# Kernel tuning notes

Measured on AMD Instinct MI355X. Metric: run time of the kernel, lower is better.

The kernel has to match this reference:

```python
import jax, jax.numpy as jnp
from jax import lax
import numpy as np

B, T, E, D, U = 64, 2048, 512, 1024, 128


def setup_inputs() -> dict:
    key = jax.random.key(0)
    ks = jax.random.split(key, 12)
    s = 0.05
    queries = jax.random.normal(ks[0], (B, 1, D), jnp.float32)
    prev = jax.random.uniform(ks[1], (B, T), jnp.float32)
    prev = prev / prev.sum(-1, keepdims=True)  # alignment-like (sums to 1)
    enc = jax.random.normal(ks[2], (B, T, E), jnp.float32)
    lengths = jax.random.randint(ks[3], (B,), 1, T + 1)
    conv_w = jax.random.normal(ks[4], (U, 1, 3), jnp.float32) * s   # (out,in,k)
    conv_b = jax.random.normal(ks[5], (U,), jnp.float32) * s
    Wq = jax.random.normal(ks[6], (U, D), jnp.float32) * s          # query_layer weight
    Wk = jax.random.normal(ks[7], (U, E), jnp.float32) * s          # key_layer weight
    v_w = jax.random.normal(ks[8], (1, U), jnp.float32) * s         # v weight
    v_b = jax.random.normal(ks[9], (1,), jnp.float32) * s           # v bias
    b = jax.random.uniform(ks[10], (U,), jnp.float32)               # nn.Parameter(torch.rand)
    return dict(queries=queries, previous_alignments=prev, encoder_output=enc,
                conv_w=conv_w, conv_b=conv_b, Wq=Wq, Wk=Wk, v_w=v_w, v_b=v_b,
                b=b, lengths=lengths)


def reference(queries, previous_alignments, encoder_output, conv_w, conv_b,
              Wq, Wk, v_w, v_b, b, lengths):
    Bt, Tt, Et = encoder_output.shape
    # set_memory: proj_key and mask
    proj_key = jnp.einsum('bte,ue->btu', encoder_output, Wk)          # (B,T,U)
    mask = jnp.arange(Tt)[None, :] >= lengths[:, None]                # (B,T)
    # conv1d on previous alignments, kernel 3, padding 1
    conv = lax.conv_general_dilated(previous_alignments[:, None, :], conv_w,
                                    window_strides=(1,), padding=[(1, 1)],
                                    dimension_numbers=('NCH', 'OIH', 'NCH'))
    conv_attn = (conv + conv_b[None, :, None]).transpose(0, 2, 1)     # (B,T,U)
    q_proj = jnp.einsum('bqd,ud->bqu', queries, Wq)                   # (B,1,U)
    w = jnp.tanh(q_proj + proj_key + conv_attn + b)                   # (B,T,U)
    score = jnp.einsum('btu,u->bt', w, v_w[0]) + v_b[0]               # (B,T)
    score = jnp.where(mask, -jnp.inf, score)
    attn_weight = jax.nn.softmax(score, axis=-1)                      # (B,T)
    context = jnp.einsum('bt,bte->be', attn_weight, encoder_output)[:, None, :]  # (B,1,E)
    return context, attn_weight
```

## Files before the change

### kernel.cpp

```cpp
#include <hip/hip_runtime.h>
#include <hip/hip_bf16.h>

typedef __bf16 bf16x8 __attribute__((ext_vector_type(8)));
typedef float  f32x4  __attribute__((ext_vector_type(4)));

#define Bsz 64
#define Tdim 2048
#define Edim 512
#define Ddim 1024
#define Udim 128
#define CHUNK 128
#define NCHUNK 16

__device__ inline unsigned short f2bf(float f) {
    union { float f; unsigned int u; } x{f};
    unsigned int r = x.u + 0x7FFFu + ((x.u >> 16) & 1u);
    return (unsigned short)(r >> 16);
}

__device__ inline float fast_tanh(float x) {
    float e = __expf(2.f * x);
    return 1.f - __fdividef(2.f, e + 1.f);
}

__global__ __launch_bounds__(256) void k_prep(const float* __restrict__ q,
                                              const float* __restrict__ Wq,
                                              const float* __restrict__ bparam,
                                              const float* __restrict__ convb,
                                              const float* __restrict__ Wk,
                                              unsigned short* __restrict__ wkbf,
                                              float* __restrict__ qb) {
    int bid = blockIdx.x, tid = threadIdx.x;
    if (bid >= 512) {
        int cb = bid - 512;
        #pragma unroll
        for (int k = 0; k < 4; ++k) {
            int i = (((cb * 4 + k) * 256) + tid) * 4;
            float4 v = *reinterpret_cast<const float4*>(Wk + i);
            ushort4 h = make_ushort4(f2bf(v.x), f2bf(v.y), f2bf(v.z), f2bf(v.w));
            *reinterpret_cast<ushort4*>(wkbf + i) = h;
        }
        return;
    }
    int wg   = bid * 4 + (tid >> 6);
    int lane = tid & 63;
    int b  = wg >> 5;
    int u0 = (wg & 31) * 4;
    const float* qr = q + (size_t)b * Ddim + lane * 16;
    float4 qv[4];
    #pragma unroll
    for (int i = 0; i < 4; ++i) qv[i] = *reinterpret_cast<const float4*>(qr + i * 4);
    float s[4];
    #pragma unroll
    for (int jj = 0; jj < 4; ++jj) {
        const float* wr = Wq + (size_t)(u0 + jj) * Ddim + lane * 16;
        float acc = 0.f;
        #pragma unroll
        for (int i = 0; i < 4; ++i) {
            float4 w = *reinterpret_cast<const float4*>(wr + i * 4);
            acc += qv[i].x * w.x + qv[i].y * w.y + qv[i].z * w.z + qv[i].w * w.w;
        }
        s[jj] = acc;
    }
    #pragma unroll
    for (int m = 32; m; m >>= 1) {
        #pragma unroll
        for (int jj = 0; jj < 4; ++jj) s[jj] += __shfl_xor(s[jj], m);
    }
    if (lane == 0) {
        #pragma unroll
        for (int jj = 0; jj < 4; ++jj)
            qb[b * 128 + u0 + jj] = s[jj] + bparam[u0 + jj] + convb[u0 + jj];
    }
}

__global__ __launch_bounds__(256) void k_score_ctx(const float* __restrict__ enc,
                                                   const float* __restrict__ prev,
                                                   const unsigned short* __restrict__ wkbf,
                                                   const float* __restrict__ qb,
                                                   const float* __restrict__ conv_w,
                                                   const float* __restrict__ v_w,
                                                   const float* __restrict__ v_b,
                                                   const int* __restrict__ lengths,
                                                   float* __restrict__ score_out,
                                                   float* __restrict__ m_ws,
                                                   float* __restrict__ l_ws,
                                                   float* __restrict__ c_ws) {
    __shared__ alignas(16) unsigned short At[128 * 64];
    __shared__ alignas(16) unsigned short Bt[128 * 64];
    __shared__ float s_prev[130];
    __shared__ float s_qb[128];
    __shared__ float s_vw[128];
    __shared__ float s_cw[3][128];
    __shared__ float s_score[128];
    __shared__ float s_p[128];
    __shared__ alignas(16) float s_cred[128 * 4];

    const int tid   = threadIdx.x;
    const int b     = blockIdx.y;
    const int chunk = blockIdx.x;
    const int t0    = chunk * CHUNK;
    const int lane  = tid & 63, wid = tid >> 6;
    const int len   = lengths[b];
    const int pidx  = b * NCHUNK + chunk;

    if (t0 >= len) {
        if (tid == 0) { m_ws[pidx] = -3.4e38f; l_ws[pidx] = 0.f; }
        return;
    }

    if (tid < 128) {
        s_qb[tid]    = qb[b * 128 + tid];
        s_vw[tid]    = v_w[tid];
        s_cw[0][tid] = conv_w[tid * 3 + 0];
        s_cw[1][tid] = conv_w[tid * 3 + 1];
        s_cw[2][tid] = conv_w[tid * 3 + 2];
    }
    if (tid < 130) {
        int idx = t0 - 1 + tid;
        s_prev[tid] = (idx >= 0 && idx < Tdim) ? prev[b * Tdim + idx] : 0.f;
    }

    const float* encb = enc + ((size_t)b * Tdim + t0) * Edim;

    f32x4 acc[2][8];
    #pragma unroll
    for (int m2 = 0; m2 < 2; ++m2)
        #pragma unroll
        for (int n = 0; n < 8; ++n) acc[m2][n] = (f32x4){0.f, 0.f, 0.f, 0.f};

    for (int e0 = 0; e0 < Edim; e0 += 64) {
        #pragma unroll
        for (int i = 0; i < 8; ++i) {
            int lin = tid + i * 256;
            int r = lin >> 4, c4 = lin & 15;
            float4 v = *reinterpret_cast<const float4*>(encb + (size_t)r * Edim + e0 + c4 * 4);
            ushort4 h = make_ushort4(f2bf(v.x), f2bf(v.y), f2bf(v.z), f2bf(v.w));
            int off = (r * 128 + c4 * 8) ^ ((r & 7) << 4);
            *reinterpret_cast<ushort4*>(reinterpret_cast<char*>(At) + off) = h;
        }
        #pragma unroll
        for (int i = 0; i < 4; ++i) {
            int lin = tid + i * 256;
            int u = lin >> 3, c8 = lin & 7;
            uint4 w = *reinterpret_cast<const uint4*>(wkbf + (size_t)u * Edim + e0 + c8 * 8);
            int off = (u * 128 + c8 * 16) ^ ((u & 7) << 4);
            *reinterpret_cast<uint4*>(reinterpret_cast<char*>(Bt) + off) = w;
        }
        __syncthreads();
        #pragma unroll
        for (int kk = 0; kk < 2; ++kk) {
            #pragma unroll
            for (int m2 = 0; m2 < 2; ++m2) {
                int ar = wid * 32 + m2 * 16 + (lane & 15);
                int abyte = (ar * 128 + kk * 64 + (lane >> 4) * 16) ^ ((ar & 7) << 4);
                bf16x8 af = *reinterpret_cast<const bf16x8*>(reinterpret_cast<const char*>(At) + abyte);
                #pragma unroll
                for (int n = 0; n < 8; ++n) {
                    int br = n * 16 + (lane & 15);
                    int bbyte = (br * 128 + kk * 64 + (lane >> 4) * 16) ^ ((br & 7) << 4);
                    bf16x8 bv = *reinterpret_cast<const bf16x8*>(reinterpret_cast<const char*>(Bt) + bbyte);
                    acc[m2][n] = __builtin_amdgcn_mfma_f32_16x16x32_bf16(af, bv, acc[m2][n], 0, 0, 0);
                }
            }
        }
        __syncthreads();
    }

    float sc[2][4] = {{0.f,0.f,0.f,0.f},{0.f,0.f,0.f,0.f}};
    #pragma unroll
    for (int m2 = 0; m2 < 2; ++m2) {
        #pragma unroll
        for (int n = 0; n < 8; ++n) {
            int u = n * 16 + (lane & 15);
            float c0 = s_cw[0][u], c1 = s_cw[1][u], c2 = s_cw[2][u];
            float qbu = s_qb[u], vwu = s_vw[u];
            #pragma unroll
            for (int j = 0; j < 4; ++j) {
                int tl = wid * 32 + m2 * 16 + (lane >> 4) * 4 + j;
                float conv = s_prev[tl] * c0 + s_prev[tl + 1] * c1 + s_prev[tl + 2] * c2;
                sc[m2][j] += vwu * fast_tanh(acc[m2][n][j] + qbu + conv);
            }
        }
    }
    #pragma unroll
    for (int m2 = 0; m2 < 2; ++m2)
        #pragma unroll
        for (int j = 0; j < 4; ++j) {
            sc[m2][j] += __shfl_xor(sc[m2][j], 1);
            sc[m2][j] += __shfl_xor(sc[m2][j], 2);
            sc[m2][j] += __shfl_xor(sc[m2][j], 4);
            sc[m2][j] += __shfl_xor(sc[m2][j], 8);
        }
    if ((lane & 15) == 0) {
        float vb = v_b[0];
        #pragma unroll
        for (int m2 = 0; m2 < 2; ++m2) {
            int tl = wid * 32 + m2 * 16 + (lane >> 4) * 4;
            #pragma unroll
            for (int j = 0; j < 4; ++j) {
                float s = sc[m2][j] + vb;
                s_score[tl + j] = s;
                score_out[b * Tdim + t0 + tl + j] = s;
            }
        }
    }
    __syncthreads();

    float sv0 = (t0 + lane < len)      ? s_score[lane]      : -3.4e38f;
    float sv1 = (t0 + 64 + lane < len) ? s_score[lane + 64] : -3.4e38f;
    float m = fmaxf(sv0, sv1);
    #pragma unroll
    for (int s = 32; s; s >>= 1) m = fmaxf(m, __shfl_xor(m, s));
    float p0 = (t0 + lane < len)      ? __expf(sv0 - m) : 0.f;
    float p1 = (t0 + 64 + lane < len) ? __expf(sv1 - m) : 0.f;
    float l = p0 + p1;
    #pragma unroll
    for (int s = 32; s; s >>= 1) l += __shfl_xor(l, s);
    if (tid < 64) { s_p[tid] = p0; s_p[tid + 64] = p1; }
    if (tid == 0) { m_ws[pidx] = m; l_ws[pidx] = l; }
    __syncthreads();

    {
        int e4 = (tid & 127) * 4;
        int th = tid >> 7;
        float4 a = make_float4(0.f, 0.f, 0.f, 0.f);
        #pragma unroll 4
        for (int t = th; t < CHUNK; t += 2) {
            float pt = s_p[t];
            float4 v = *reinterpret_cast<const float4*>(encb + (size_t)t * Edim + e4);
            a.x += pt * v.x; a.y += pt * v.y; a.z += pt * v.z; a.w += pt * v.w;
        }
        if (th == 1) *reinterpret_cast<float4*>(&s_cred[(tid & 127) * 4]) = a;
        __syncthreads();
        if (th == 0) {
            float4 o = *reinterpret_cast<const float4*>(&s_cred[tid * 4]);
            a.x += o.x; a.y += o.y; a.z += o.z; a.w += o.w;
            *reinterpret_cast<float4*>(c_ws + (size_t)pidx * Edim + e4) = a;
        }
    }
}

__global__ __launch_bounds__(256) void k_combine(const float* __restrict__ m_ws,
                                                 const float* __restrict__ l_ws,
                                                 const float* __restrict__ c_ws,
                                                 const int* __restrict__ lengths,
                                                 float* __restrict__ ctx,
                                                 float* __restrict__ attn) {
    int b = blockIdx.x, tid = threadIdx.x;
    int lane = tid & 63, wid = tid >> 6;
    __shared__ float s_w[NCHUNK];
    __shared__ float sM, sinvL;

    if (wid == 0) {
        float mj = (lane < NCHUNK) ? m_ws[b * NCHUNK + lane] : -3.4e38f;
        float lj = (lane < NCHUNK) ? l_ws[b * NCHUNK + lane] : 0.f;
        float M = mj;
        #pragma unroll
        for (int s = 32; s; s >>= 1) M = fmaxf(M, __shfl_xor(M, s));
        float w = (lj > 0.f) ? __expf(mj - M) : 0.f;
        float L = lj * w;
        #pragma unroll
        for (int s = 32; s; s >>= 1) L += __shfl_xor(L, s);
        if (lane < NCHUNK) s_w[lane] = w;
        if (lane == 0) { sM = M; sinvL = 1.f / L; }
    }
    __syncthreads();
    float M = sM, invL = sinvL;

    {
        int e2 = tid * 2;
        float ax = 0.f, ay = 0.f;
        #pragma unroll 4
        for (int j = 0; j < NCHUNK; ++j) {
            float w = s_w[j];
            if (w != 0.f) {
                float2 v = *reinterpret_cast<const float2*>(c_ws + ((size_t)(b * NCHUNK + j)) * Edim + e2);
                ax += w * v.x; ay += w * v.y;
            }
        }
        float2 r = make_float2(ax * invL, ay * invL);
        *reinterpret_cast<float2*>(ctx + (size_t)b * Edim + e2) = r;
    }

    int len = lengths[b];
    #pragma unroll
    for (int i = 0; i < Tdim / 256; ++i) {
        int t = tid + i * 256;
        float s = attn[(size_t)b * Tdim + t];
        attn[(size_t)b * Tdim + t] = (t < len) ? __expf(s - M) * invL : 0.f;
    }
}

extern "C" void kernel_launch(void* const* d_in, const int* in_sizes, int n_in,
                              void* d_out, int out_size, void* d_ws, size_t ws_size,
                              hipStream_t stream) {
    const float* queries = (const float*)d_in[0];
    const float* prev    = (const float*)d_in[1];
    const float* enc     = (const float*)d_in[2];
    const float* conv_w  = (const float*)d_in[3];
    const float* conv_b  = (const float*)d_in[4];
    const float* Wq      = (const float*)d_in[5];
    const float* Wk      = (const float*)d_in[6];
    const float* v_w     = (const float*)d_in[7];
    const float* v_b     = (const float*)d_in[8];
    const float* bparam  = (const float*)d_in[9];
    const int*   lengths = (const int*)d_in[10];

    float* out  = (float*)d_out;
    float* ctx  = out;
    float* attn = out + Bsz * Edim;

    char* ws = (char*)d_ws;
    unsigned short* wkbf = (unsigned short*)ws;
    float* qb   = (float*)(ws + 131072);
    float* m_ws = (float*)(ws + 163840);
    float* l_ws = (float*)(ws + 172032);
    float* c_ws = (float*)(ws + 196608);

    k_prep<<<528, 256, 0, stream>>>(queries, Wq, bparam, conv_b, Wk, wkbf, qb);
    k_score_ctx<<<dim3(NCHUNK, Bsz), 256, 0, stream>>>(enc, prev, wkbf, qb, conv_w, v_w, v_b,
                                                       lengths, attn, m_ws, l_ws, c_ws);
    k_combine<<<Bsz, 256, 0, stream>>>(m_ws, l_ws, c_ws, lengths, ctx, attn);
}
```

Measured before the change: 80.35 us.

## Double time chunk per block and use native bf16 conversions

Each score/context block now covers 256 time steps instead of 128, with a 4x8 MFMA accumulator tile per wave. This halves the number of blocks and the redundant Wk tile staging per time step. The manual round-to-nearest bf16 bit trick is replaced by native __bf16 casts, which can map to hardware convert instructions. The prep kernel's query projection now computes 8 units per wave with fewer blocks. The cost is more registers per thread and coarser skipping of masked chunks, which may reduce occupancy and add wasted work past each sequence length.

```diff
diff --git a/kernel.cpp b/kernel.cpp
--- a/kernel.cpp
+++ b/kernel.cpp
@@ -2,6 +2,7 @@
 #include <hip/hip_bf16.h>
 
 typedef __bf16 bf16x8 __attribute__((ext_vector_type(8)));
+typedef __bf16 bf16x4 __attribute__((ext_vector_type(4)));
 typedef float  f32x4  __attribute__((ext_vector_type(4)));
 
 #define Bsz 64
@@ -9,13 +10,13 @@
 #define Edim 512
 #define Ddim 1024
 #define Udim 128
-#define CHUNK 128
-#define NCHUNK 16
-
-__device__ inline unsigned short f2bf(float f) {
-    union { float f; unsigned int u; } x{f};
-    unsigned int r = x.u + 0x7FFFu + ((x.u >> 16) & 1u);
-    return (unsigned short)(r >> 16);
+#define CHUNK 256
+#define NCHUNK 8
+
+__device__ inline bf16x4 cvt4(float4 v) {
+    bf16x4 h;
+    h[0] = (__bf16)v.x; h[1] = (__bf16)v.y; h[2] = (__bf16)v.z; h[3] = (__bf16)v.w;
+    return h;
 }
 
 __device__ inline float fast_tanh(float x) {
@@ -31,28 +32,27 @@
                                               unsigned short* __restrict__ wkbf,
                                               float* __restrict__ qb) {
     int bid = blockIdx.x, tid = threadIdx.x;
-    if (bid >= 512) {
-        int cb = bid - 512;
+    if (bid >= 256) {
+        int cb = bid - 256;
         #pragma unroll
         for (int k = 0; k < 4; ++k) {
             int i = (((cb * 4 + k) * 256) + tid) * 4;
             float4 v = *reinterpret_cast<const float4*>(Wk + i);
-            ushort4 h = make_ushort4(f2bf(v.x), f2bf(v.y), f2bf(v.z), f2bf(v.w));
-            *reinterpret_cast<ushort4*>(wkbf + i) = h;
+            *reinterpret_cast<bf16x4*>(wkbf + i) = cvt4(v);
         }
         return;
     }
     int wg   = bid * 4 + (tid >> 6);
     int lane = tid & 63;
-    int b  = wg >> 5;
-    int u0 = (wg & 31) * 4;
+    int b  = wg >> 4;
+    int u0 = (wg & 15) * 8;
     const float* qr = q + (size_t)b * Ddim + lane * 16;
     float4 qv[4];
     #pragma unroll
     for (int i = 0; i < 4; ++i) qv[i] = *reinterpret_cast<const float4*>(qr + i * 4);
-    float s[4];
-    #pragma unroll
-    for (int jj = 0; jj < 4; ++jj) {
+    float s[8];
+    #pragma unroll
+    for (int jj = 0; jj < 8; ++jj) {
         const float* wr = Wq + (size_t)(u0 + jj) * Ddim + lane * 16;
         float acc = 0.f;
         #pragma unroll
@@ -65,11 +65,11 @@
     #pragma unroll
     for (int m = 32; m; m >>= 1) {
         #pragma unroll
-        for (int jj = 0; jj < 4; ++jj) s[jj] += __shfl_xor(s[jj], m);
+        for (int jj = 0; jj < 8; ++jj) s[jj] += __shfl_xor(s[jj], m);
     }
     if (lane == 0) {
         #pragma unroll
-        for (int jj = 0; jj < 4; ++jj)
+        for (int jj = 0; jj < 8; ++jj)
             qb[b * 128 + u0 + jj] = s[jj] + bparam[u0 + jj] + convb[u0 + jj];
     }
 }
@@ -86,14 +86,14 @@
                                                    float* __restrict__ m_ws,
                                                    float* __restrict__ l_ws,
                                                    float* __restrict__ c_ws) {
-    __shared__ alignas(16) unsigned short At[128 * 64];
+    __shared__ alignas(16) unsigned short At[256 * 64];
     __shared__ alignas(16) unsigned short Bt[128 * 64];
-    __shared__ float s_prev[130];
+    __shared__ float s_prev[258];
     __shared__ float s_qb[128];
     __shared__ float s_vw[128];
     __shared__ float s_cw[3][128];
-    __shared__ float s_score[128];
-    __shared__ float s_p[128];
+    __shared__ float s_score[256];
+    __shared__ float s_p[256];
     __shared__ alignas(16) float s_cred[128 * 4];
 
     const int tid   = threadIdx.x;
@@ -116,28 +116,32 @@
         s_cw[1][tid] = conv_w[tid * 3 + 1];
         s_cw[2][tid] = conv_w[tid * 3 + 2];
     }
-    if (tid < 130) {
+    if (tid < 258 - 128 && tid + 128 < 258) {}
+    if (tid < 258) {
         int idx = t0 - 1 + tid;
         s_prev[tid] = (idx >= 0 && idx < Tdim) ? prev[b * Tdim + idx] : 0.f;
     }
+    if (tid < 2) {
+        int idx = t0 - 1 + 256 + tid;
+        s_prev[256 + tid] = (idx >= 0 && idx < Tdim) ? prev[b * Tdim + idx] : 0.f;
+    }
 
     const float* encb = enc + ((size_t)b * Tdim + t0) * Edim;
 
-    f32x4 acc[2][8];
-    #pragma unroll
-    for (int m2 = 0; m2 < 2; ++m2)
+    f32x4 acc[4][8];
+    #pragma unroll
+    for (int m2 = 0; m2 < 4; ++m2)
         #pragma unroll
         for (int n = 0; n < 8; ++n) acc[m2][n] = (f32x4){0.f, 0.f, 0.f, 0.f};
 
     for (int e0 = 0; e0 < Edim; e0 += 64) {
         #pragma unroll
-        for (int i = 0; i < 8; ++i) {
+        for (int i = 0; i < 16; ++i) {
             int lin = tid + i * 256;
             int r = lin >> 4, c4 = lin & 15;
             float4 v = *reinterpret_cast<const float4*>(encb + (size_t)r * Edim + e0 + c4 * 4);
-            ushort4 h = make_ushort4(f2bf(v.x), f2bf(v.y), f2bf(v.z), f2bf(v.w));
             int off = (r * 128 + c4 * 8) ^ ((r & 7) << 4);
-            *reinterpret_cast<ushort4*>(reinterpret_cast<char*>(At) + off) = h;
+            *reinterpret_cast<bf16x4*>(reinterpret_cast<char*>(At) + off) = cvt4(v);
         }
         #pragma unroll
         for (int i = 0; i < 4; ++i) {
@@ -151,8 +155,8 @@
         #pragma unroll
         for (int kk = 0; kk < 2; ++kk) {
             #pragma unroll
-            for (int m2 = 0; m2 < 2; ++m2) {
-                int ar = wid * 32 + m2 * 16 + (lane & 15);
+            for (int m2 = 0; m2 < 4; ++m2) {
+                int ar = wid * 64 + m2 * 16 + (lane & 15);
                 int abyte = (ar * 128 + kk * 64 + (lane >> 4) * 16) ^ ((ar & 7) << 4);
                 bf16x8 af = *reinterpret_cast<const bf16x8*>(reinterpret_cast<const char*>(At) + abyte);
                 #pragma unroll
@@ -167,9 +171,13 @@
         __syncthreads();
     }
 
-    float sc[2][4] = {{0.f,0.f,0.f,0.f},{0.f,0.f,0.f,0.f}};
-    #pragma unroll
-    for (int m2 = 0; m2 < 2; ++m2) {
+    float sc[4][4];
+    #pragma unroll
+    for (int m2 = 0; m2 < 4; ++m2)
+        #pragma unroll
+        for (int j = 0; j < 4; ++j) sc[m2][j] = 0.f;
+    #pragma unroll
+    for (int m2 = 0; m2 < 4; ++m2) {
         #pragma unroll
         for (int n = 0; n < 8; ++n) {
             int u = n * 16 + (lane & 15);
@@ -177,14 +185,14 @@
             float qbu = s_qb[u], vwu = s_vw[u];
             #pragma unroll
             for (int j = 0; j < 4; ++j) {
-                int tl = wid * 32 + m2 * 16 + (lane >> 4) * 4 + j;
+                int tl = wid * 64 + m2 * 16 + (lane >> 4) * 4 + j;
                 float conv = s_prev[tl] * c0 + s_prev[tl + 1] * c1 + s_prev[tl + 2] * c2;
                 sc[m2][j] += vwu * fast_tanh(acc[m2][n][j] + qbu + conv);
             }
         }
     }
     #pragma unroll
-    for (int m2 = 0; m2 < 2; ++m2)
+    for (int m2 = 0; m2 < 4; ++m2)
         #pragma unroll
         for (int j = 0; j < 4; ++j) {
             sc[m2][j] += __shfl_xor(sc[m2][j], 1);
@@ -195,8 +203,8 @@
     if ((lane & 15) == 0) {
         float vb = v_b[0];
         #pragma unroll
-        for (int m2 = 0; m2 < 2; ++m2) {
-            int tl = wid * 32 + m2 * 16 + (lane >> 4) * 4;
+        for (int m2 = 0; m2 < 4; ++m2) {
+            int tl = wid * 64 + m2 * 16 + (lane >> 4) * 4;
             #pragma unroll
             for (int j = 0; j < 4; ++j) {
                 float s = sc[m2][j] + vb;
@@ -207,17 +215,27 @@
     }
     __syncthreads();
 
-    float sv0 = (t0 + lane < len)      ? s_score[lane]      : -3.4e38f;
-    float sv1 = (t0 + 64 + lane < len) ? s_score[lane + 64] : -3.4e38f;
-    float m = fmaxf(sv0, sv1);
+    float sv[4], pv[4];
+    float m = -3.4e38f;
+    #pragma unroll
+    for (int h = 0; h < 4; ++h) {
+        sv[h] = (t0 + h * 64 + lane < len) ? s_score[h * 64 + lane] : -3.4e38f;
+        m = fmaxf(m, sv[h]);
+    }
     #pragma unroll
     for (int s = 32; s; s >>= 1) m = fmaxf(m, __shfl_xor(m, s));
-    float p0 = (t0 + lane < len)      ? __expf(sv0 - m) : 0.f;
-    float p1 = (t0 + 64 + lane < len) ? __expf(sv1 - m) : 0.f;
-    float l = p0 + p1;
+    float l = 0.f;
+    #pragma unroll
+    for (int h = 0; h < 4; ++h) {
+        pv[h] = (t0 + h * 64 + lane < len) ? __expf(sv[h] - m) : 0.f;
+        l += pv[h];
+    }
     #pragma unroll
     for (int s = 32; s; s >>= 1) l += __shfl_xor(l, s);
-    if (tid < 64) { s_p[tid] = p0; s_p[tid + 64] = p1; }
+    if (tid < 64) {
+        #pragma unroll
+        for (int h = 0; h < 4; ++h) s_p[h * 64 + tid] = pv[h];
+    }
     if (tid == 0) { m_ws[pidx] = m; l_ws[pidx] = l; }
     __syncthreads();
 
@@ -271,7 +289,7 @@
     {
         int e2 = tid * 2;
         float ax = 0.f, ay = 0.f;
-        #pragma unroll 4
+        #pragma unroll
         for (int j = 0; j < NCHUNK; ++j) {
             float w = s_w[j];
             if (w != 0.f) {
@@ -318,7 +336,7 @@
     float* l_ws = (float*)(ws + 172032);
     float* c_ws = (float*)(ws + 196608);
 
-    k_prep<<<528, 256, 0, stream>>>(queries, Wq, bparam, conv_b, Wk, wkbf, qb);
+    k_prep<<<272, 256, 0, stream>>>(queries, Wq, bparam, conv_b, Wk, wkbf, qb);
     k_score_ctx<<<dim3(NCHUNK, Bsz), 256, 0, stream>>>(enc, prev, wkbf, qb, conv_w, v_w, v_b,
                                                        lengths, attn, m_ws, l_ws, c_ws);
     k_combine<<<Bsz, 256, 0, stream>>>(m_ws, l_ws, c_ws, lengths, ctx, attn);
```

New measurement: 108.7 us. 1.35x slower.

## Pre-swizzle Wk into MFMA fragment layout and read B operands from global

Applied to the files above, without the earlier changes.

The prep kernel now writes the bf16 copy of Wk directly in the per-lane MFMA B-fragment order. The score kernel loads B fragments straight from global/L2 instead of staging them in shared memory, which removes the Bt LDS buffer and its stores. Encoder loads are widened to 8 floats per thread with compiler bf16 conversion, and the q-projection uses 8 outputs per wave. This saves LDS traffic and space but depends on L2 hits for the repeated Wk fragment reads across blocks.

```diff
diff --git a/kernel.cpp b/kernel.cpp
--- a/kernel.cpp
+++ b/kernel.cpp
@@ -2,6 +2,7 @@
 #include <hip/hip_bf16.h>
 
 typedef __bf16 bf16x8 __attribute__((ext_vector_type(8)));
+typedef __bf16 bf16x4 __attribute__((ext_vector_type(4)));
 typedef float  f32x4  __attribute__((ext_vector_type(4)));
 
 #define Bsz 64
@@ -12,10 +13,16 @@
 #define CHUNK 128
 #define NCHUNK 16
 
-__device__ inline unsigned short f2bf(float f) {
-    union { float f; unsigned int u; } x{f};
-    unsigned int r = x.u + 0x7FFFu + ((x.u >> 16) & 1u);
-    return (unsigned short)(r >> 16);
+__device__ inline bf16x4 cvt4(float4 v) {
+    bf16x4 h;
+    h[0] = (__bf16)v.x; h[1] = (__bf16)v.y; h[2] = (__bf16)v.z; h[3] = (__bf16)v.w;
+    return h;
+}
+__device__ inline bf16x8 cvt8(float4 a, float4 b) {
+    bf16x8 h;
+    h[0] = (__bf16)a.x; h[1] = (__bf16)a.y; h[2] = (__bf16)a.z; h[3] = (__bf16)a.w;
+    h[4] = (__bf16)b.x; h[5] = (__bf16)b.y; h[6] = (__bf16)b.z; h[7] = (__bf16)b.w;
+    return h;
 }
 
 __device__ inline float fast_tanh(float x) {
@@ -31,28 +38,35 @@
                                               unsigned short* __restrict__ wkbf,
                                               float* __restrict__ qb) {
     int bid = blockIdx.x, tid = threadIdx.x;
-    if (bid >= 512) {
-        int cb = bid - 512;
-        #pragma unroll
-        for (int k = 0; k < 4; ++k) {
-            int i = (((cb * 4 + k) * 256) + tid) * 4;
-            float4 v = *reinterpret_cast<const float4*>(Wk + i);
-            ushort4 h = make_ushort4(f2bf(v.x), f2bf(v.y), f2bf(v.z), f2bf(v.w));
-            *reinterpret_cast<ushort4*>(wkbf + i) = h;
+    if (bid >= 256) {
+        int cb = bid - 256;
+        #pragma unroll
+        for (int k = 0; k < 2; ++k) {
+            int E = (cb * 256 + tid) * 2 + k;
+            int l  = E & 63;
+            int n  = (E >> 6) & 7;
+            int kk = (E >> 9) & 1;
+            int es = E >> 10;
+            int u  = n * 16 + (l & 15);
+            int e  = es * 64 + kk * 32 + (l >> 4) * 8;
+            const float* src = Wk + (size_t)u * Edim + e;
+            float4 a = *reinterpret_cast<const float4*>(src);
+            float4 b = *reinterpret_cast<const float4*>(src + 4);
+            *reinterpret_cast<bf16x8*>(wkbf + (size_t)E * 8) = cvt8(a, b);
         }
         return;
     }
     int wg   = bid * 4 + (tid >> 6);
     int lane = tid & 63;
-    int b  = wg >> 5;
-    int u0 = (wg & 31) * 4;
+    int b  = wg >> 4;
+    int u0 = (wg & 15) * 8;
     const float* qr = q + (size_t)b * Ddim + lane * 16;
     float4 qv[4];
     #pragma unroll
     for (int i = 0; i < 4; ++i) qv[i] = *reinterpret_cast<const float4*>(qr + i * 4);
-    float s[4];
-    #pragma unroll
-    for (int jj = 0; jj < 4; ++jj) {
+    float s[8];
+    #pragma unroll
+    for (int jj = 0; jj < 8; ++jj) {
         const float* wr = Wq + (size_t)(u0 + jj) * Ddim + lane * 16;
         float acc = 0.f;
         #pragma unroll
@@ -65,11 +79,11 @@
     #pragma unroll
     for (int m = 32; m; m >>= 1) {
         #pragma unroll
-        for (int jj = 0; jj < 4; ++jj) s[jj] += __shfl_xor(s[jj], m);
+        for (int jj = 0; jj < 8; ++jj) s[jj] += __shfl_xor(s[jj], m);
     }
     if (lane == 0) {
         #pragma unroll
-        for (int jj = 0; jj < 4; ++jj)
+        for (int jj = 0; jj < 8; ++jj)
             qb[b * 128 + u0 + jj] = s[jj] + bparam[u0 + jj] + convb[u0 + jj];
     }
 }
@@ -87,7 +101,6 @@
                                                    float* __restrict__ l_ws,
                                                    float* __restrict__ c_ws) {
     __shared__ alignas(16) unsigned short At[128 * 64];
-    __shared__ alignas(16) unsigned short Bt[128 * 64];
     __shared__ float s_prev[130];
     __shared__ float s_qb[128];
     __shared__ float s_vw[128];
@@ -122,6 +135,7 @@
     }
 
     const float* encb = enc + ((size_t)b * Tdim + t0) * Edim;
+    const unsigned short* wb = wkbf + lane * 8;
 
     f32x4 acc[2][8];
     #pragma unroll
@@ -129,39 +143,37 @@
         #pragma unroll
         for (int n = 0; n < 8; ++n) acc[m2][n] = (f32x4){0.f, 0.f, 0.f, 0.f};
 
-    for (int e0 = 0; e0 < Edim; e0 += 64) {
-        #pragma unroll
-        for (int i = 0; i < 8; ++i) {
-            int lin = tid + i * 256;
-            int r = lin >> 4, c4 = lin & 15;
-            float4 v = *reinterpret_cast<const float4*>(encb + (size_t)r * Edim + e0 + c4 * 4);
-            ushort4 h = make_ushort4(f2bf(v.x), f2bf(v.y), f2bf(v.z), f2bf(v.w));
-            int off = (r * 128 + c4 * 8) ^ ((r & 7) << 4);
-            *reinterpret_cast<ushort4*>(reinterpret_cast<char*>(At) + off) = h;
-        }
+    for (int es = 0; es < 8; ++es) {
+        const int e0 = es * 64;
         #pragma unroll
         for (int i = 0; i < 4; ++i) {
             int lin = tid + i * 256;
-            int u = lin >> 3, c8 = lin & 7;
-            uint4 w = *reinterpret_cast<const uint4*>(wkbf + (size_t)u * Edim + e0 + c8 * 8);
-            int off = (u * 128 + c8 * 16) ^ ((u & 7) << 4);
-            *reinterpret_cast<uint4*>(reinterpret_cast<char*>(Bt) + off) = w;
+            int r = lin >> 3, c8 = lin & 7;
+            const float* src = encb + (size_t)r * Edim + e0 + c8 * 8;
+            float4 va = *reinterpret_cast<const float4*>(src);
+            float4 vb2 = *reinterpret_cast<const float4*>(src + 4);
+            int off = (r * 128 + c8 * 16) ^ ((r & 7) << 4);
+            *reinterpret_cast<bf16x8*>(reinterpret_cast<char*>(At) + off) = cvt8(va, vb2);
         }
         __syncthreads();
         #pragma unroll
         for (int kk = 0; kk < 2; ++kk) {
+            bf16x8 af[2];
             #pragma unroll
             for (int m2 = 0; m2 < 2; ++m2) {
                 int ar = wid * 32 + m2 * 16 + (lane & 15);
                 int abyte = (ar * 128 + kk * 64 + (lane >> 4) * 16) ^ ((ar & 7) << 4);
-                bf16x8 af = *reinterpret_cast<const bf16x8*>(reinterpret_cast<const char*>(At) + abyte);
-                #pragma unroll
-                for (int n = 0; n < 8; ++n) {
-                    int br = n * 16 + (lane & 15);
-                    int bbyte = (br * 128 + kk * 64 + (lane >> 4) * 16) ^ ((br & 7) << 4);
-                    bf16x8 bv = *reinterpret_cast<const bf16x8*>(reinterpret_cast<const char*>(Bt) + bbyte);
-                    acc[m2][n] = __builtin_amdgcn_mfma_f32_16x16x32_bf16(af, bv, acc[m2][n], 0, 0, 0);
-                }
+                af[m2] = *reinterpret_cast<const bf16x8*>(reinterpret_cast<const char*>(At) + abyte);
+            }
+            const unsigned short* wkk = wb + (size_t)((es * 2 + kk) * 8) * 512;
+            bf16x8 bv[8];
+            #pragma unroll
+            for (int n = 0; n < 8; ++n)
+                bv[n] = *reinterpret_cast<const bf16x8*>(wkk + (size_t)n * 512);
+            #pragma unroll
+            for (int n = 0; n < 8; ++n) {
+                acc[0][n] = __builtin_amdgcn_mfma_f32_16x16x32_bf16(af[0], bv[n], acc[0][n], 0, 0, 0);
+                acc[1][n] = __builtin_amdgcn_mfma_f32_16x16x32_bf16(af[1], bv[n], acc[1][n], 0, 0, 0);
             }
         }
         __syncthreads();
@@ -271,7 +283,7 @@
     {
         int e2 = tid * 2;
         float ax = 0.f, ay = 0.f;
-        #pragma unroll 4
+        #pragma unroll
         for (int j = 0; j < NCHUNK; ++j) {
             float w = s_w[j];
             if (w != 0.f) {
@@ -318,7 +330,7 @@
     float* l_ws = (float*)(ws + 172032);
     float* c_ws = (float*)(ws + 196608);
 
-    k_prep<<<528, 256, 0, stream>>>(queries, Wq, bparam, conv_b, Wk, wkbf, qb);
+    k_prep<<<272, 256, 0, stream>>>(queries, Wq, bparam, conv_b, Wk, wkbf, qb);
     k_score_ctx<<<dim3(NCHUNK, Bsz), 256, 0, stream>>>(enc, prev, wkbf, qb, conv_w, v_w, v_b,
                                                        lengths, attn, m_ws, l_ws, c_ws);
     k_combine<<<Bsz, 256, 0, stream>>>(m_ws, l_ws, c_ws, lengths, ctx, attn);
```

New measurement: 104.0 us. 29.5% more time.
